# Kernel optimization log

Hardware: AMD Instinct MI355X
Metric: run time of the kernel (lower is better)

Reference implementation:

```python
import jax, jax.numpy as jnp
import numpy as np

HIDDEN = 2048
HEADS = 16
HEAD_DIM = HIDDEN // HEADS
ROPE_BASE = 10000.0


def rope_cos_sin(seq_len, dim, dtype=jnp.float32):
    inv_freq = 1.0 / (ROPE_BASE ** (jnp.arange(0, dim, 2, dtype=jnp.float32) / dim))
    t = jnp.arange(seq_len, dtype=jnp.float32)
    freqs = jnp.einsum('i,j->ij', t, inv_freq)            # [S, dim/2]
    emb = jnp.concatenate([freqs, freqs], axis=-1)        # [S, dim]
    return jnp.cos(emb).astype(dtype), jnp.sin(emb).astype(dtype)


def rotate_half(x):
    x1, x2 = jnp.split(x, 2, axis=-1)
    return jnp.concatenate([-x2, x1], axis=-1)


def setup_inputs() -> dict:
    key = jax.random.key(0)
    ks = jax.random.split(key, 6)
    B, S, D = 2, 2048, HIDDEN
    scale = 1.0 / np.sqrt(D)
    x = jax.random.normal(ks[0], (B, S, D), dtype=jnp.float32)
    Wq = jax.random.normal(ks[1], (D, D), dtype=jnp.float32) * scale
    Wk = jax.random.normal(ks[2], (D, D), dtype=jnp.float32) * scale
    Wv = jax.random.normal(ks[3], (D, D), dtype=jnp.float32) * scale
    Wo = jax.random.normal(ks[4], (D, D), dtype=jnp.float32) * scale
    bo = jnp.zeros((D,), dtype=jnp.float32)
    return {"x": x, "Wq": Wq, "Wk": Wk, "Wv": Wv, "Wo": Wo, "bo": bo}


def reference(x, Wq, Wk, Wv, Wo, bo):
    B, S, D = x.shape
    H, Dh = HEADS, HEAD_DIM
    # torch Linear: x @ W.T
    q = (x @ Wq.T).reshape(B, S, H, Dh).transpose(0, 2, 1, 3)  # [B,H,S,Dh]
    k = (x @ Wk.T).reshape(B, S, H, Dh).transpose(0, 2, 1, 3)
    v = (x @ Wv.T).reshape(B, S, H, Dh).transpose(0, 2, 1, 3)
    cos, sin = rope_cos_sin(S, Dh, x.dtype)                    # [S, Dh]
    q = q * cos + rotate_half(q) * sin
    k = k * cos + rotate_half(k) * sin
    scale = Dh ** -0.5
    attn = jnp.einsum('bhqd,bhkd->bhqk', q, k) * scale
    attn = jax.nn.softmax(attn, axis=-1)
    out = jnp.einsum('bhqk,bhkd->bhqd', attn, v)               # [B,H,S,Dh]
    out = out.transpose(0, 2, 1, 3).reshape(B, S, D)
    return out @ Wo.T + bo
```

## Files before the change

### kernel.cpp

```cpp
#include <hip/hip_runtime.h>
#include <stdint.h>


#define SEQ 2048
#define HD 128
#define DMODEL 2048

typedef __bf16 bf16x8 __attribute__((ext_vector_type(8)));
typedef float f32x4 __attribute__((ext_vector_type(4)));
typedef unsigned short u16;
typedef unsigned int u32;

typedef bf16x8 __attribute__((may_alias)) bf16x8_a;
typedef uint2 __attribute__((may_alias)) uint2_a;
typedef uint4 __attribute__((may_alias)) uint4_a;

__device__ __forceinline__ u16 f2bf(float f) {
  unsigned int u = __float_as_uint(f);
  u += 0x7fff + ((u >> 16) & 1);
  return (u16)(u >> 16);
}

typedef __attribute__((address_space(1))) void* gas_t;
typedef __attribute__((address_space(3))) void* las_t;
__device__ __forceinline__ void load_lds16(const void* g, void* l) {
  __builtin_amdgcn_global_load_lds((gas_t)(uintptr_t)g,
                                   (las_t)(uint32_t)(uintptr_t)l, 16, 0, 0);
}

__global__ void conv_all(const float* __restrict__ x,
                         const float* __restrict__ wq,
                         const float* __restrict__ wk,
                         const float* __restrict__ wv,
                         const float* __restrict__ wo,
                         u16* __restrict__ xb, u16* __restrict__ wqkv,
                         u16* __restrict__ wob) {
  int i = blockIdx.x * 256 + threadIdx.x;
  const float* src;
  u16* dst;
  int off;
  if (i < 2097152) { src = x; dst = xb; off = i; }
  else if (i < 3145728) { src = wq; dst = wqkv; off = i - 2097152; }
  else if (i < 4194304) { src = wk; dst = wqkv + 4194304; off = i - 3145728; }
  else if (i < 5242880) { src = wv; dst = wqkv + 8388608; off = i - 4194304; }
  else { src = wo; dst = wob; off = i - 5242880; }
  float4 v = ((const float4*)src)[off];
  ushort4 o;
  o.x = f2bf(v.x); o.y = f2bf(v.y); o.z = f2bf(v.z); o.w = f2bf(v.w);
  ((ushort4*)dst)[off] = o;
}

template <bool SWAP>
__device__ __forceinline__ void gemm_core(
    const u16* __restrict__ A, const u16* __restrict__ Bm, int row0, int col0,
    int K, u16* Asl, u16* Bsl, int wave, int lane, int quad, int l15,
    int waveM, int waveN, f32x4 acc[4][4]) {
  for (int k0 = 0; k0 < K; k0 += 64) {
    __syncthreads();
#pragma unroll
    for (int j = 0; j < 4; ++j) {
      int idx = (wave * 4 + j) * 64 + lane;
      int r = idx >> 3;
      int c8 = (idx & 7) ^ (r & 7);
      load_lds16(A + (size_t)(row0 + r) * K + (k0 + c8 * 8), &Asl[idx * 8]);
      load_lds16(Bm + (size_t)(col0 + r) * K + (k0 + c8 * 8), &Bsl[idx * 8]);
    }
    __syncthreads();
#pragma unroll
    for (int c = 0; c < 2; ++c) {
      bf16x8 af[4], bfr[4];
#pragma unroll
      for (int mt = 0; mt < 4; ++mt) {
        int r = waveM + mt * 16 + l15;
        af[mt] = *(const bf16x8*)&Asl[(r * 8 + ((c * 4 + quad) ^ (r & 7))) * 8];
      }
#pragma unroll
      for (int nt = 0; nt < 4; ++nt) {
        int r = waveN + nt * 16 + l15;
        bfr[nt] = *(const bf16x8*)&Bsl[(r * 8 + ((c * 4 + quad) ^ (r & 7))) * 8];
      }
#pragma unroll
      for (int mt = 0; mt < 4; ++mt)
#pragma unroll
        for (int nt = 0; nt < 4; ++nt) {
          if (SWAP)
            acc[mt][nt] = __builtin_amdgcn_mfma_f32_16x16x32_bf16(
                bfr[nt], af[mt], acc[mt][nt], 0, 0, 0);
          else
            acc[mt][nt] = __builtin_amdgcn_mfma_f32_16x16x32_bf16(
                af[mt], bfr[nt], acc[mt][nt], 0, 0, 0);
        }
    }
  }
}


#define BARR asm volatile("s_barrier" ::: "memory")
#define LGKM0 asm volatile("s_waitcnt lgkmcnt(0)" ::: "memory")
#define VMW4 asm volatile("s_waitcnt vmcnt(4)" ::: "memory")
#define VMW0 asm volatile("s_waitcnt vmcnt(0)" ::: "memory")

#define STG(OP, DB, HF, KOFF) do {                                          \
    const u16* gb_ = ((OP) ? Bg : Ag) + (HF) * 262144 + (KOFF);             \
    u16* lb_ = S + ((OP) ? 32768 : 0) + (DB) * 16384 + (HF) * 8192;         \
    load_lds16(gb_ + off0, lb_ + tid * 8);                                  \
    load_lds16(gb_ + off1, lb_ + (tid + 512) * 8);                          \
  } while (0)

#define LDA(DB, MH) do {                                                    \
    const u16* ab_ = S + (DB) * 16384 + wm * 8192;                          \
    _Pragma("unroll") for (int mt_ = 0; mt_ < 4; ++mt_) {                   \
      int rA_ = (MH) * 64 + mt_ * 16 + l15;                                 \
      int sw_ = rA_ & 7;                                                    \
      af[mt_][0] = *(const bf16x8_a*)(ab_ + (rA_ * 8 + (quad ^ sw_)) * 8);  \
      af[mt_][1] = *(const bf16x8_a*)(ab_ + (rA_ * 8 + ((4 + quad) ^ sw_)) * 8); \
    } } while (0)

#define LDB(DB, NH, DST) do {                                               \
    const u16* bb_ = S + 32768 + (DB) * 16384 + (wn >> 1) * 8192;           \
    _Pragma("unroll") for (int nt_ = 0; nt_ < 2; ++nt_) {                   \
      int rB_ = (wn & 1) * 64 + (NH) * 32 + nt_ * 16 + l15;                 \
      int sw_ = rB_ & 7;                                                    \
      DST[nt_][0] = *(const bf16x8_a*)(bb_ + (rB_ * 8 + (quad ^ sw_)) * 8); \
      DST[nt_][1] = *(const bf16x8_a*)(bb_ + (rB_ * 8 + ((4 + quad) ^ sw_)) * 8); \
    } } while (0)

#define MMQ(MH, NH, BFR) do {                                               \
    __builtin_amdgcn_s_setprio(1);                                          \
    _Pragma("unroll") for (int c_ = 0; c_ < 2; ++c_)                        \
      _Pragma("unroll") for (int mt_ = 0; mt_ < 4; ++mt_)                   \
        _Pragma("unroll") for (int nt_ = 0; nt_ < 2; ++nt_) {               \
          if (VM)                                                           \
            acc[(MH) * 4 + mt_][(NH) * 2 + nt_] =                           \
                __builtin_amdgcn_mfma_f32_16x16x32_bf16(                    \
                    BFR[nt_][c_], af[mt_][c_],                              \
                    acc[(MH) * 4 + mt_][(NH) * 2 + nt_], 0, 0, 0);          \
          else                                                              \
            acc[(MH) * 4 + mt_][(NH) * 2 + nt_] =                           \
                __builtin_amdgcn_mfma_f32_16x16x32_bf16(                    \
                    af[mt_][c_], BFR[nt_][c_],                              \
                    acc[(MH) * 4 + mt_][(NH) * 2 + nt_], 0, 0, 0);          \
        }                                                                   \
    __builtin_amdgcn_s_setprio(0);                                          \
  } while (0)

template <bool VM>
__device__ __forceinline__ void qkv_core(const u16* __restrict__ Ag,
                                         const u16* __restrict__ Bg,
                                         u16* __restrict__ S, int tid,
                                         f32x4 acc[8][4]) {
  const int lane = tid & 63;
  const int wave = tid >> 6;
  const int quad = lane >> 4;
  const int l15 = lane & 15;
  const int wm = wave >> 2;
  const int wn = wave & 3;

  const int r0_ = tid >> 3;
  const u32 off0 = (u32)r0_ * 2048u + (u32)(((tid & 7) ^ (r0_ & 7)) * 8);
  const int i1_ = tid + 512;
  const int r1_ = i1_ >> 3;
  const u32 off1 = (u32)r1_ * 2048u + (u32)(((i1_ & 7) ^ (r1_ & 7)) * 8);

  bf16x8 af[4][2], bn0[2][2], bn1[2][2];

  STG(1, 0, 0, 0);
  STG(0, 0, 0, 0);
  STG(0, 0, 1, 0);
  STG(1, 0, 1, 0);
  STG(1, 1, 0, 64);
  STG(1, 1, 1, 64);
  VMW4;
  BARR;

#pragma unroll 1
  for (int kb = 0; kb < 1920; kb += 128) {
    LDA(0, 0); LDB(0, 0, bn0); STG(0, 1, 0, kb + 64);
    BARR; LGKM0; MMQ(0, 0, bn0); BARR;
    LDB(0, 1, bn1); STG(0, 1, 1, kb + 64);
    BARR; LGKM0; MMQ(0, 1, bn1); BARR;
    LDA(0, 1); STG(1, 0, 0, kb + 128);
    BARR; LGKM0; MMQ(1, 0, bn0); BARR;
    STG(0, 0, 0, kb + 128);
    BARR; MMQ(1, 1, bn1); VMW4; BARR;
    LDA(1, 0); LDB(1, 0, bn0); STG(0, 0, 1, kb + 128);
    BARR; LGKM0; MMQ(0, 0, bn0); BARR;
    LDB(1, 1, bn1); STG(1, 0, 1, kb + 128);
    BARR; LGKM0; MMQ(0, 1, bn1); BARR;
    LDA(1, 1); STG(1, 1, 0, kb + 192);
    BARR; LGKM0; MMQ(1, 0, bn0); BARR;
    STG(1, 1, 1, kb + 192);
    BARR; MMQ(1, 1, bn1); VMW4; BARR;
  }

  LDA(0, 0); LDB(0, 0, bn0); STG(0, 1, 0, 1984);
  BARR; LGKM0; MMQ(0, 0, bn0); BARR;
  LDB(0, 1, bn1); STG(0, 1, 1, 1984);
  BARR; LGKM0; MMQ(0, 1, bn1); BARR;
  LDA(0, 1);
  BARR; LGKM0; MMQ(1, 0, bn0); BARR;
  BARR; MMQ(1, 1, bn1); VMW0; BARR;
  LDA(1, 0); LDB(1, 0, bn0);
  BARR; LGKM0; MMQ(0, 0, bn0); BARR;
  LDB(1, 1, bn1);
  BARR; LGKM0; MMQ(0, 1, bn1); BARR;
  LDA(1, 1);
  BARR; LGKM0; MMQ(1, 0, bn0); BARR;
  BARR; MMQ(1, 1, bn1); BARR;
}

#undef STG
#undef LDA
#undef LDB
#undef MMQ

__global__ __launch_bounds__(512, 2)
void gemm_qkv(const u16* __restrict__ A, const u16* __restrict__ Bm,
              u16* __restrict__ qkv, u16* __restrict__ vt) {
  __shared__ __align__(16) u16 S[65536];

  const int tid = threadIdx.x;
  int orig = blockIdx.y * 24 + blockIdx.x;
  int swz = (orig & 7) * 48 + (orig >> 3);
  const int bx = swz % 24;
  const int by = swz / 24;
  const int row0 = by * 256;
  const int col0 = bx * 256;
  const bool vmode = bx >= 16;

  const u16* Ag = A + (size_t)row0 * 2048;
  const u16* Bg = Bm + (size_t)col0 * 2048;

  f32x4 acc[8][4] = {};
  if (vmode) qkv_core<true>(Ag, Bg, S, tid, acc);
  else       qkv_core<false>(Ag, Bg, S, tid, acc);

  const int lane = tid & 63;
  const int wave = tid >> 6;
  const int quad = lane >> 4;
  const int l15 = lane & 15;
  const int wm = wave >> 2;
  const int wn = wave & 3;

  const int which = col0 >> 11;
  const float qs = (which == 0) ? 0.12751744f : 1.0f;

#pragma unroll
  for (int mh = 0; mh < 2; ++mh)
#pragma unroll
    for (int nh = 0; nh < 2; ++nh)
#pragma unroll
      for (int mt = 0; mt < 4; ++mt)
#pragma unroll
        for (int nt = 0; nt < 2; ++nt)
#pragma unroll
          for (int r = 0; r < 4; ++r) {
            int el;
            if (vmode) {
              int dd = wn * 64 + nh * 32 + nt * 16 + quad * 4 + r;
              int ss = wm * 128 + mh * 64 + mt * 16 + l15;
              el = dd * 256 + (((ss >> 3) ^ (dd & 31)) * 8) + (ss & 7);
            } else {
              int ss = wm * 128 + mh * 64 + mt * 16 + quad * 4 + r;
              int dd = wn * 64 + nh * 32 + nt * 16 + l15;
              el = ss * 256 + (((dd >> 3) ^ (ss & 31)) * 8) + (dd & 7);
            }
            S[el] = f2bf(acc[mh * 4 + mt][nh * 2 + nt][r] * qs);
          }
  __syncthreads();

  const int a = lane & 7;
  const int sg = lane >> 3;
  const int h0 = (col0 >> 7) & 15;
  const int brow = row0 >> 11;
  const int sbase = row0 & 2047;

  if (!vmode) {
    const float c1 = 0.2076205059304601f;
    const float c2 = 2.6514961294723187f;
#pragma unroll
    for (int pass = 0; pass < 4; ++pass) {
      int s_l = pass * 64 + wave * 8 + sg;
      int s2048 = sbase + s_l;
      int sw = s_l & 31;
#pragma unroll
      for (int hh = 0; hh < 2; ++hh) {
        bf16x8 x1 = *(const bf16x8_a*)&S[s_l * 256 + (((hh * 16 + a) ^ sw) * 8)];
        bf16x8 x2 = *(const bf16x8_a*)&S[s_l * 256 + (((hh * 16 + a + 8) ^ sw) * 8)];
        u16 o1[8], o2[8];
#pragma unroll
        for (int e = 0; e < 8; ++e) {
          float j = (float)(a * 8 + e);
          float rev = (float)s2048 * __builtin_amdgcn_exp2f(-c1 * j - c2);
          rev = __builtin_amdgcn_fractf(rev);
          float sn = __builtin_amdgcn_sinf(rev);
          float cs = __builtin_amdgcn_cosf(rev);
          float v1 = (float)x1[e], v2 = (float)x2[e];
          o1[e] = f2bf(v1 * cs - v2 * sn);
          o2[e] = f2bf(v2 * cs + v1 * sn);
        }
        size_t base = ((((size_t)which * 2 + brow) * 16 + (h0 + hh)) * SEQ +
                       s2048) * HD + a * 8;
        *(uint4_a*)&qkv[base] = *(uint4*)o1;
        *(uint4_a*)&qkv[base + 64] = *(uint4*)o2;
      }
    }
  } else {
#pragma unroll
    for (int pass = 0; pass < 4; ++pass) {
      int d_l = pass * 64 + wave * 8 + sg;
      int h = h0 + (d_l >> 7);
      int dw = d_l & 31;
      size_t rb = (((size_t)brow * 16 + h) * HD + (d_l & 127)) * SEQ + sbase;
#pragma unroll
      for (int g = 0; g < 4; ++g) {
        int As = g * 8 + a;
        bf16x8 y = *(const bf16x8_a*)&S[d_l * 256 + ((As ^ dw) * 8)];
        *(uint4_a*)&vt[rb + As * 8] = *(uint4_a*)&y;
      }
    }
  }
}

__global__ __launch_bounds__(256, 3)
void gemm_out(const u16* __restrict__ A, const u16* __restrict__ Bm,
              float* __restrict__ C, const float* __restrict__ bias, int N,
              int K) {
  __shared__ __align__(16) u16 Smem[2][128 * 64];
  const int tid = threadIdx.x;
  const int lane = tid & 63;
  const int wave = tid >> 6;
  const int quad = lane >> 4;
  const int l15 = lane & 15;
  const int row0 = blockIdx.y * 128;
  const int col0 = blockIdx.x * 128;
  const int waveM = (wave & 1) * 64;
  const int waveN = (wave >> 1) * 64;

  f32x4 acc[4][4] = {};
  gemm_core<false>(A, Bm, row0, col0, K, Smem[0], Smem[1], wave, lane, quad,
                   l15, waveM, waveN, acc);

#pragma unroll
  for (int nt = 0; nt < 4; ++nt) {
    int d = col0 + waveN + nt * 16 + l15;
    float bv = bias[d];
#pragma unroll
    for (int mt = 0; mt < 4; ++mt) {
#pragma unroll
      for (int r = 0; r < 4; ++r) {
        int row = row0 + waveM + mt * 16 + quad * 4 + r;
        C[(size_t)row * N + d] = acc[mt][nt][r] + bv;
      }
    }
  }
}

__global__ __launch_bounds__(256, 2)
void attn_kernel(const u16* __restrict__ qkv, const u16* __restrict__ vt,
                 u16* __restrict__ attn_out) {
  __shared__ __align__(16) u16 Kl[64 * 128];
  __shared__ __align__(16) u16 Vl[128 * 64];
  __shared__ __align__(16) u16 Pl[4][32 * 64];

  const int tid = threadIdx.x;
  const int lane = tid & 63;
  const int wave = tid >> 6;
  const int quad = lane >> 4;
  const int l15 = lane & 15;
  const int q0 = blockIdx.x * 128;
  const int bh = blockIdx.y;
  const size_t SD = (size_t)SEQ * HD;

  const u16* Q = qkv + (size_t)bh * SD;
  const u16* Kg = qkv + (size_t)(32 + bh) * SD;
  const u16* Vg = vt + (size_t)bh * SD;

  bf16x8 onesf;
#pragma unroll
  for (int e = 0; e < 8; ++e)
    onesf[e] = (l15 == 0) ? (__bf16)1.0f : (__bf16)0.0f;

  bf16x8 qf[2][4];
#pragma unroll
  for (int mt = 0; mt < 2; ++mt) {
    int qrow = q0 + wave * 32 + mt * 16 + l15;
#pragma unroll
    for (int c = 0; c < 4; ++c)
      qf[mt][c] = *(const bf16x8*)(Q + (size_t)qrow * HD + c * 32 + quad * 8);
  }

  f32x4 of[9][2] = {};
  u16* pw = &Pl[wave][0];

  for (int kv0 = 0; kv0 < SEQ; kv0 += 64) {
    __syncthreads();
#pragma unroll
    for (int j = 0; j < 4; ++j) {
      int idx = (wave * 4 + j) * 64 + lane;
      {
        int r = idx >> 4, cs = idx & 15;
        int cc = cs ^ (r & 15);
        load_lds16(Kg + (size_t)(kv0 + r) * HD + cc * 8, &Kl[idx * 8]);
      }
      {
        int r = idx >> 3, cs = idx & 7;
        int cc = cs ^ (r & 7);
        load_lds16(Vg + (size_t)r * SEQ + kv0 + cc * 8, &Vl[idx * 8]);
      }
    }
    __syncthreads();

    f32x4 sc[4][2] = {};
#pragma unroll
    for (int c = 0; c < 4; ++c) {
      bf16x8 kf[4];
#pragma unroll
      for (int nt = 0; nt < 4; ++nt)
        kf[nt] = *(const bf16x8*)&Kl[((nt * 16 + l15) * 16 +
                                      ((c * 4 + quad) ^ l15)) * 8];
#pragma unroll
      for (int nt = 0; nt < 4; ++nt)
#pragma unroll
        for (int mt = 0; mt < 2; ++mt)
          sc[nt][mt] = __builtin_amdgcn_mfma_f32_16x16x32_bf16(
              kf[nt], qf[mt][c], sc[nt][mt], 0, 0, 0);
    }

#pragma unroll
    for (int nt = 0; nt < 4; ++nt) {
#pragma unroll
      for (int mt = 0; mt < 2; ++mt) {
        float p0 = __builtin_amdgcn_exp2f(sc[nt][mt][0]);
        float p1 = __builtin_amdgcn_exp2f(sc[nt][mt][1]);
        float p2 = __builtin_amdgcn_exp2f(sc[nt][mt][2]);
        float p3 = __builtin_amdgcn_exp2f(sc[nt][mt][3]);
        u32 lo = __builtin_amdgcn_perm(__float_as_uint(p1),
                                       __float_as_uint(p0), 0x07060302u);
        u32 hi = __builtin_amdgcn_perm(__float_as_uint(p3),
                                       __float_as_uint(p2), 0x07060302u);
        int row = mt * 16 + l15;
        int a = nt * 2 + (quad >> 1);
        int idx16 = (row * 8 + (a ^ (l15 & 7))) * 8 + (quad & 1) * 4;
        uint2 pk; pk.x = lo; pk.y = hi;
        *(uint2_a*)&pw[idx16] = pk;
      }
    }

#pragma unroll
    for (int c = 0; c < 2; ++c) {
      bf16x8 pf[2];
#pragma unroll
      for (int mt = 0; mt < 2; ++mt)
        pf[mt] = *(const bf16x8_a*)&pw[((mt * 16 + l15) * 8 +
                                        ((c * 4 + quad) ^ (l15 & 7))) * 8];
#pragma unroll
      for (int dt = 0; dt < 9; ++dt) {
        bf16x8 vf = (dt < 8)
                        ? *(const bf16x8*)&Vl[((dt * 16 + l15) * 8 +
                                               ((c * 4 + quad) ^ (l15 & 7))) * 8]
                        : onesf;
#pragma unroll
        for (int mt = 0; mt < 2; ++mt)
          of[dt][mt] = __builtin_amdgcn_mfma_f32_16x16x32_bf16(
              vf, pf[mt], of[dt][mt], 0, 0, 0);
      }
    }
  }

  const int b = bh >> 4, h = bh & 15;
#pragma unroll
  for (int mt = 0; mt < 2; ++mt) {
    float lsum = __shfl(of[8][mt][0], l15, 64);
    float inv = 1.f / lsum;
    int s = q0 + wave * 32 + mt * 16 + l15;
    size_t rowb = ((size_t)b * SEQ + s) * DMODEL + h * HD;
#pragma unroll
    for (int dt = 0; dt < 8; ++dt) {
      ushort4 ov;
      ov.x = f2bf(of[dt][mt][0] * inv);
      ov.y = f2bf(of[dt][mt][1] * inv);
      ov.z = f2bf(of[dt][mt][2] * inv);
      ov.w = f2bf(of[dt][mt][3] * inv);
      *(ushort4*)&attn_out[rowb + dt * 16 + quad * 4] = ov;
    }
  }
}

extern "C" void kernel_launch(void* const* d_in, const int* in_sizes, int n_in,
                              void* d_out, int out_size, void* d_ws,
                              size_t ws_size, hipStream_t stream) {
  const float* x = (const float*)d_in[0];
  const float* Wq = (const float*)d_in[1];
  const float* Wk = (const float*)d_in[2];
  const float* Wv = (const float*)d_in[3];
  const float* Wo = (const float*)d_in[4];
  const float* bo = (const float*)d_in[5];
  float* out = (float*)d_out;

  char* ws = (char*)d_ws;
  u16* xb = (u16*)(ws);
  u16* wqkv = (u16*)(ws + (size_t)(16 << 20));
  u16* wob = (u16*)(ws + (size_t)(40 << 20));
  u16* qkv = (u16*)(ws + (size_t)(48 << 20));
  u16* vt = qkv + (size_t)2 * 8388608;
  u16* attn = xb;

  conv_all<<<24576, 256, 0, stream>>>(x, Wq, Wk, Wv, Wo, xb, wqkv, wob);

  gemm_qkv<<<dim3(24, 16), 512, 0, stream>>>(xb, wqkv, qkv, vt);
  attn_kernel<<<dim3(16, 32), 256, 0, stream>>>(qkv, vt, attn);
  gemm_out<<<dim3(16, 32), 256, 0, stream>>>(attn, wob, out, bo, 2048, 2048);
}
```

Measured before the change: 373.3 us.

## Double-buffer K/V tiles in attention kernel with async prefetch and MFMA priority

The attention kernel now keeps two LDS buffers for the K and V tiles and prefetches tile t+2 while tile t is being computed. Waits use vmcnt counters instead of full syncthreads around every load, so global-to-LDS traffic can overlap the MFMA work. s_setprio is raised around the MFMA sections to favour matrix issue. The cost is twice the K/V LDS footprint (about 80KB total), which may limit two blocks per CU. The correctness of the wait counts also depends on the exact number of outstanding loads per stage.

Measured after the change: 363.0 us. 2.7% less time.

```diff
diff --git a/kernel.cpp b/kernel.cpp
--- a/kernel.cpp
+++ b/kernel.cpp
@@ -94,10 +94,10 @@
   }
 }
 
-
 #define BARR asm volatile("s_barrier" ::: "memory")
 #define LGKM0 asm volatile("s_waitcnt lgkmcnt(0)" ::: "memory")
 #define VMW4 asm volatile("s_waitcnt vmcnt(4)" ::: "memory")
+#define VMW8 asm volatile("s_waitcnt vmcnt(8)" ::: "memory")
 #define VMW0 asm volatile("s_waitcnt vmcnt(0)" ::: "memory")
 
 #define STG(OP, DB, HF, KOFF) do {                                          \
@@ -359,8 +359,8 @@
 __global__ __launch_bounds__(256, 2)
 void attn_kernel(const u16* __restrict__ qkv, const u16* __restrict__ vt,
                  u16* __restrict__ attn_out) {
-  __shared__ __align__(16) u16 Kl[64 * 128];
-  __shared__ __align__(16) u16 Vl[128 * 64];
+  __shared__ __align__(16) u16 Kl[2][64 * 128];
+  __shared__ __align__(16) u16 Vl[2][128 * 64];
   __shared__ __align__(16) u16 Pl[4][32 * 64];
 
   const int tid = threadIdx.x;
@@ -393,31 +393,42 @@
   f32x4 of[9][2] = {};
   u16* pw = &Pl[wave][0];
 
-  for (int kv0 = 0; kv0 < SEQ; kv0 += 64) {
-    __syncthreads();
+  auto stage = [&](int tile, int buf) {
+    int kv0 = tile * 64;
 #pragma unroll
     for (int j = 0; j < 4; ++j) {
       int idx = (wave * 4 + j) * 64 + lane;
       {
         int r = idx >> 4, cs = idx & 15;
         int cc = cs ^ (r & 15);
-        load_lds16(Kg + (size_t)(kv0 + r) * HD + cc * 8, &Kl[idx * 8]);
+        load_lds16(Kg + (size_t)(kv0 + r) * HD + cc * 8, &Kl[buf][idx * 8]);
       }
       {
         int r = idx >> 3, cs = idx & 7;
         int cc = cs ^ (r & 7);
-        load_lds16(Vg + (size_t)r * SEQ + kv0 + cc * 8, &Vl[idx * 8]);
-      }
-    }
-    __syncthreads();
+        load_lds16(Vg + (size_t)r * SEQ + kv0 + cc * 8, &Vl[buf][idx * 8]);
+      }
+    }
+  };
+
+  stage(0, 0);
+  stage(1, 1);
+  VMW8;
+  BARR;
+
+#pragma unroll 2
+  for (int t = 0; t < 32; ++t) {
+    const u16* Kb = Kl[t & 1];
+    const u16* Vb = Vl[t & 1];
 
     f32x4 sc[4][2] = {};
+    __builtin_amdgcn_s_setprio(1);
 #pragma unroll
     for (int c = 0; c < 4; ++c) {
       bf16x8 kf[4];
 #pragma unroll
       for (int nt = 0; nt < 4; ++nt)
-        kf[nt] = *(const bf16x8*)&Kl[((nt * 16 + l15) * 16 +
+        kf[nt] = *(const bf16x8*)&Kb[((nt * 16 + l15) * 16 +
                                       ((c * 4 + quad) ^ l15)) * 8];
 #pragma unroll
       for (int nt = 0; nt < 4; ++nt)
@@ -426,6 +437,7 @@
           sc[nt][mt] = __builtin_amdgcn_mfma_f32_16x16x32_bf16(
               kf[nt], qf[mt][c], sc[nt][mt], 0, 0, 0);
     }
+    __builtin_amdgcn_s_setprio(0);
 
 #pragma unroll
     for (int nt = 0; nt < 4; ++nt) {
@@ -447,6 +459,7 @@
       }
     }
 
+    __builtin_amdgcn_s_setprio(1);
 #pragma unroll
     for (int c = 0; c < 2; ++c) {
       bf16x8 pf[2];
@@ -457,7 +470,7 @@
 #pragma unroll
       for (int dt = 0; dt < 9; ++dt) {
         bf16x8 vf = (dt < 8)
-                        ? *(const bf16x8*)&Vl[((dt * 16 + l15) * 8 +
+                        ? *(const bf16x8*)&Vb[((dt * 16 + l15) * 8 +
                                                ((c * 4 + quad) ^ (l15 & 7))) * 8]
                         : onesf;
 #pragma unroll
@@ -466,6 +479,16 @@
               vf, pf[mt], of[dt][mt], 0, 0, 0);
       }
     }
+    __builtin_amdgcn_s_setprio(0);
+
+    BARR;
+    if (t < 30) {
+      stage(t + 2, t & 1);
+      VMW8;
+    } else {
+      VMW0;
+    }
+    BARR;
   }
 
   const int b = bh >> 4, h = bh & 15;
```
